# Kernel optimization log

Measured on AMD Instinct MI355X. Metric: run time of the kernel, lower is better.

The kernel has to match this reference:

```python
import jax, jax.numpy as jnp
import numpy as np

WEIGHT_BITS = 4           # weight_bit_width for both convs
SCALE_MIN = 2e-16         # scaling_min_val from CommonIntWeightPerTensorQuant


def fake_quant_per_channel(w, bits):
    """Brevitas-style per-output-channel symmetric narrow-range int fake quant.
    scale = max|w| over each output channel / (2^(bits-1) - 1), STE round."""
    qmax = float(2 ** (bits - 1) - 1)
    absmax = jnp.max(jnp.abs(w.reshape(w.shape[0], -1)), axis=1)
    scale = jnp.maximum(absmax / qmax, SCALE_MIN)
    scale = scale.reshape((-1,) + (1,) * (w.ndim - 1))
    q = jnp.clip(jnp.round(w / scale), -qmax, qmax) * scale
    # straight-through estimator (matches brevitas round_ste)
    return w + jax.lax.stop_gradient(q - w)


def setup_inputs() -> dict:
    key = jax.random.key(0)
    k1, k2, k3, k4 = jax.random.split(key, 4)
    x = jax.random.normal(k1, (32, 384, 56, 56), dtype=jnp.float32)
    # depthwise weight: (out=C, in/groups=1, kH, kW)
    dw_w = jax.random.normal(k2, (384, 1, 3, 3), dtype=jnp.float32) * 0.1
    # pointwise weight: (out, in, 1, 1); pw conv has default bias=True
    pw_w = jax.random.normal(k3, (384, 384, 1, 1), dtype=jnp.float32) * 0.05
    pw_b = jax.random.normal(k4, (384,), dtype=jnp.float32) * 0.01
    return {"x": x, "dw_w": dw_w, "pw_w": pw_w, "pw_b": pw_b}


def reference(x, dw_w, pw_w, pw_b):
    C = dw_w.shape[0]
    dw_q = fake_quant_per_channel(dw_w, WEIGHT_BITS)
    pw_q = fake_quant_per_channel(pw_w, WEIGHT_BITS)
    # depthwise 3x3, stride 1, pad 1
    y = jax.lax.conv_general_dilated(
        x, dw_q, window_strides=(1, 1), padding=((1, 1), (1, 1)),
        dimension_numbers=("NCHW", "OIHW", "NCHW"), feature_group_count=C)
    # pointwise 1x1 + bias
    z = jax.lax.conv_general_dilated(
        y, pw_q, window_strides=(1, 1), padding="VALID",
        dimension_numbers=("NCHW", "OIHW", "NCHW"))
    return z + pw_b[None, :, None, None]
```

## Files before the change

kernel.cpp:

```cpp
#include <hip/hip_runtime.h>
#include <hip/hip_bf16.h>

#define CCH 384
#define HW2 3136
#define HH 56
#define WW 56
#define QMAX 7.0f
#define SCALE_MIN 2e-16f
#define PB 49
#define YSLAB 512
#define YPB 24576

typedef _Float16 half8 __attribute__((ext_vector_type(8)));
typedef float f32x4 __attribute__((ext_vector_type(4)));

#define GLOAD_LDS16(g, l) __builtin_amdgcn_global_load_lds( \
    (const __attribute__((address_space(1))) void*)(g), \
    (__attribute__((address_space(3))) void*)(l), 16, 0, 0)


__global__ void quant_dw(const float* __restrict__ dw, float* __restrict__ dwq) {
    int c = blockIdx.x * blockDim.x + threadIdx.x;
    if (c >= CCH) return;
    float w[9];
    float amax = 0.f;
    #pragma unroll
    for (int j = 0; j < 9; ++j) {
        w[j] = dw[c * 9 + j];
        amax = fmaxf(amax, fabsf(w[j]));
    }
    float scale = fmaxf(amax / QMAX, SCALE_MIN);
    #pragma unroll
    for (int j = 0; j < 9; ++j) {
        float q = rintf(w[j] / scale);
        q = fminf(fmaxf(q, -QMAX), QMAX);
        dwq[c * 9 + j] = q * scale;
    }
}

__global__ void quant_pw(const float* __restrict__ pw, _Float16* __restrict__ wpk) {
    int co = blockIdx.x;
    int lane = threadIdx.x;
    float w[6];
    float amax = 0.f;
    #pragma unroll
    for (int j = 0; j < 6; ++j) {
        w[j] = pw[co * CCH + lane + j * 64];
        amax = fmaxf(amax, fabsf(w[j]));
    }
    #pragma unroll
    for (int off = 32; off >= 1; off >>= 1)
        amax = fmaxf(amax, __shfl_xor(amax, off));
    float scale = fmaxf(amax / QMAX, SCALE_MIN);
    #pragma unroll
    for (int j = 0; j < 6; ++j) {
        int ci = lane + j * 64;
        float q = rintf(w[j] / scale);
        q = fminf(fmaxf(q, -QMAX), QMAX);
        float v = q * scale;
        int kk  = ci >> 5;
        int cis = ci & 31;
        int l   = (co & 15) | ((cis >> 3) << 4);
        int idx = (kk * 24 + (co >> 4)) * 512 + l * 8 + (cis & 7);
        wpk[idx] = (_Float16)v;
    }
}


struct G8 { float l[8], c[8], r[8]; };

__device__ __forceinline__ void dw_load(const float* __restrict__ xc,
                                        float (&xn)[8], int srow, int wl) {
    if ((unsigned)srow < (unsigned)HH) {
        #pragma unroll
        for (int ch = 0; ch < 8; ++ch)
            xn[ch] = xc[(size_t)ch * HW2 + srow * WW + wl];
    } else {
        #pragma unroll
        for (int ch = 0; ch < 8; ++ch) xn[ch] = 0.f;
    }
}

__device__ __forceinline__ void dw_shuf(const float (&xn)[8], G8& g, int w) {
    #pragma unroll
    for (int ch = 0; ch < 8; ++ch) {
        float v = xn[ch];
        float xl = __shfl_up(v, 1);
        float xr = __shfl_down(v, 1);
        g.c[ch] = v;
        g.l[ch] = (w == 0) ? 0.f : xl;
        g.r[ch] = (w == WW - 1) ? 0.f : xr;
    }
}

__device__ __forceinline__ void dw_cs(const G8& ga, const G8& gb, const G8& gc,
                                      const float (&wq)[72], _Float16* yn,
                                      int orow, int w, bool act) {
    half8 hv;
    #pragma unroll
    for (int ch = 0; ch < 8; ++ch) {
        const int b = ch * 9;
        float a;
        a = ga.l[ch] * wq[b + 0];
        a = fmaf(ga.c[ch], wq[b + 1], a);
        a = fmaf(ga.r[ch], wq[b + 2], a);
        a = fmaf(gb.l[ch], wq[b + 3], a);
        a = fmaf(gb.c[ch], wq[b + 4], a);
        a = fmaf(gb.r[ch], wq[b + 5], a);
        a = fmaf(gc.l[ch], wq[b + 6], a);
        a = fmaf(gc.c[ch], wq[b + 7], a);
        a = fmaf(gc.r[ch], wq[b + 8], a);
        hv[ch] = (_Float16)a;
    }
    if (act) {
        const int pos = orow * WW + w;
        *(half8*)(yn + (size_t)(pos >> 6) * YPB + (pos & 63) * 8) = hv;
    }
}

#define DW_IT(K, RL, RS, GS, GA, GB, GC, DOLOAD)              \
    if (DOLOAD) dw_load(xc, RL, R0 + 3 + (K), wl);            \
    dw_shuf(RS, GS, w);                                       \
    dw_cs(GA, GB, GC, wq, yn, R0 + (K), w, act);

__global__ __launch_bounds__(128) void dw_kernel(
    const float* __restrict__ x, const float* __restrict__ dwq,
    _Float16* __restrict__ ypk)
{
    int bid = blockIdx.x;
    int wg = (bid & 7) * 384 + (bid >> 3);
    int uid = wg * 2 + (threadIdx.x >> 6);
    int quarter = uid & 3;
    int t2 = uid >> 2;
    int c8 = t2 % 48, n = t2 / 48;
    const int R0 = quarter * 14;

    const int w = threadIdx.x & 63;
    const int wl = w < WW ? w : WW - 1;
    const bool act = (w < WW);

    const float* xc = x + ((size_t)n * CCH + (size_t)c8 * 8) * HW2;
    _Float16* yn = ypk + (size_t)n * PB * YPB + (size_t)c8 * YSLAB;

    float wq[72];
    const float* wsrc = dwq + c8 * 72;
    #pragma unroll
    for (int i = 0; i < 72; ++i)
        wq[i] = __uint_as_float(
            __builtin_amdgcn_readfirstlane(__float_as_uint(wsrc[i])));

    float r0[8], r1[8], r2[8], r3[8];
    G8 g0, g1, g2;

    if (R0 == 0) {
        #pragma unroll
        for (int ch = 0; ch < 8; ++ch) r0[ch] = 0.f;
    } else {
        dw_load(xc, r0, R0 - 1, wl);
    }
    dw_load(xc, r1, R0, wl);
    dw_load(xc, r2, R0 + 1, wl);
    dw_load(xc, r3, R0 + 2, wl);
    dw_shuf(r0, g0, w);
    dw_shuf(r1, g1, w);

    DW_IT(0,  r0, r2, g2, g0, g1, g2, true)
    DW_IT(1,  r1, r3, g0, g1, g2, g0, true)
    DW_IT(2,  r2, r0, g1, g2, g0, g1, true)
    DW_IT(3,  r3, r1, g2, g0, g1, g2, true)
    DW_IT(4,  r0, r2, g0, g1, g2, g0, true)
    DW_IT(5,  r1, r3, g1, g2, g0, g1, true)
    DW_IT(6,  r2, r0, g2, g0, g1, g2, true)
    DW_IT(7,  r3, r1, g0, g1, g2, g0, true)
    DW_IT(8,  r0, r2, g1, g2, g0, g1, true)
    DW_IT(9,  r1, r3, g2, g0, g1, g2, true)
    DW_IT(10, r2, r0, g0, g1, g2, g0, true)
    DW_IT(11, r3, r1, g1, g2, g0, g1, true)
    DW_IT(12, r0, r2, g2, g0, g1, g2, false)
    DW_IT(13, r1, r3, g0, g1, g2, g0, false)
}


__global__ __launch_bounds__(256) void pw_kernel(
    const _Float16* __restrict__ ypk, const _Float16* __restrict__ wpk,
    const float* __restrict__ bias, float* __restrict__ out)
{
    __shared__ __align__(16) _Float16 ysh[YPB];

    int bid = blockIdx.x;
    int wg = (bid & 7) * 196 + (bid >> 3);
    int n = wg / PB, pb = wg % PB;

    const int t = threadIdx.x;
    const int lane = t & 63;
    const int g = __builtin_amdgcn_readfirstlane(t >> 6);

    const _Float16* yg = ypk + (size_t)(n * PB + pb) * YPB;
    #pragma unroll
    for (int j = 0; j < 12; ++j) {
        GLOAD_LDS16(yg + (j * 256 + t) * 8,
                    ysh + (size_t)(j * 256 + (t & 192)) * 8);
    }
    __syncthreads();

    const int lco = lane & 15;
    const int lkg = lane >> 4;
    const int cbf = g * 6;

    f32x4 acc[6][4];
    #pragma unroll
    for (int mc = 0; mc < 6; ++mc)
        #pragma unroll
        for (int np = 0; np < 4; ++np)
            acc[mc][np] = (f32x4){0.f, 0.f, 0.f, 0.f};

    for (int kk = 0; kk < 12; ++kk) {
        half8 wf[6];
        #pragma unroll
        for (int mc = 0; mc < 6; ++mc)
            wf[mc] = *(const half8*)(wpk + (size_t)(kk * 24 + cbf + mc) * 512 + lane * 8);
        half8 yf[4];
        #pragma unroll
        for (int np = 0; np < 4; ++np)
            yf[np] = *(const half8*)(ysh + kk * 2048 + lkg * 512 + (np * 16 + lco) * 8);
        #pragma unroll
        for (int mc = 0; mc < 6; ++mc)
            #pragma unroll
            for (int np = 0; np < 4; ++np)
                acc[mc][np] = __builtin_amdgcn_mfma_f32_16x16x32_f16(
                    wf[mc], yf[np], acc[mc][np], 0, 0, 0);
    }

    float* ob = out + (size_t)n * CCH * HW2 + (size_t)pb * 64;
    #pragma unroll
    for (int mc = 0; mc < 6; ++mc) {
        #pragma unroll
        for (int r = 0; r < 4; ++r) {
            const int co = g * 96 + mc * 16 + lkg * 4 + r;
            const float bv = bias[co];
            #pragma unroll
            for (int np = 0; np < 4; ++np)
                ob[(size_t)co * HW2 + np * 16 + lco] = acc[mc][np][r] + bv;
        }
    }
}


extern "C" void kernel_launch(void* const* d_in, const int* in_sizes, int n_in,
                              void* d_out, int out_size, void* d_ws, size_t ws_size,
                              hipStream_t stream) {
    const float* x  = (const float*)d_in[0];
    const float* dw = (const float*)d_in[1];
    const float* pw = (const float*)d_in[2];
    const float* pb = (const float*)d_in[3];
    float* out = (float*)d_out;

    float*    dwq = (float*)d_ws;
    _Float16* wpk = (_Float16*)(dwq + CCH * 9);
    _Float16* ypk = wpk + (size_t)CCH * CCH;

    quant_dw<<<2, 256, 0, stream>>>(dw, dwq);
    quant_pw<<<CCH, 64, 0, stream>>>(pw, wpk);

    dw_kernel<<<3072, 128, 0, stream>>>(x, dwq, ypk);
    pw_kernel<<<1568, 256, 0, stream>>>(ypk, wpk, pb, out);
}
```

Baseline: 117.7 us.

## Merge weight quant kernels and split depthwise work by channel halves instead of row quarters

Combines the two weight-quantization kernels into one launch to cut launch overhead. The depthwise kernel now has each wavefront handle 4 channels over 28 rows instead of 8 channels over 14 rows. This reduces halo-row reloads and register pressure per thread. In exchange, y stores become 8-byte writes interleaved between two wavefronts rather than single 16-byte stores.

```diff
diff --git a/kernel.cpp b/kernel.cpp
--- a/kernel.cpp
+++ b/kernel.cpp
@@ -12,6 +12,7 @@
 #define YPB 24576
 
 typedef _Float16 half8 __attribute__((ext_vector_type(8)));
+typedef _Float16 half4v __attribute__((ext_vector_type(4)));
 typedef float f32x4 __attribute__((ext_vector_type(4)));
 
 #define GLOAD_LDS16(g, l) __builtin_amdgcn_global_load_lds( \
@@ -19,71 +20,73 @@
     (__attribute__((address_space(3))) void*)(l), 16, 0, 0)
 
 
-__global__ void quant_dw(const float* __restrict__ dw, float* __restrict__ dwq) {
-    int c = blockIdx.x * blockDim.x + threadIdx.x;
-    if (c >= CCH) return;
-    float w[9];
-    float amax = 0.f;
-    #pragma unroll
-    for (int j = 0; j < 9; ++j) {
-        w[j] = dw[c * 9 + j];
-        amax = fmaxf(amax, fabsf(w[j]));
-    }
-    float scale = fmaxf(amax / QMAX, SCALE_MIN);
-    #pragma unroll
-    for (int j = 0; j < 9; ++j) {
-        float q = rintf(w[j] / scale);
-        q = fminf(fmaxf(q, -QMAX), QMAX);
-        dwq[c * 9 + j] = q * scale;
-    }
-}
-
-__global__ void quant_pw(const float* __restrict__ pw, _Float16* __restrict__ wpk) {
-    int co = blockIdx.x;
+__global__ void quant_all(const float* __restrict__ dw, const float* __restrict__ pw,
+                          float* __restrict__ dwq, _Float16* __restrict__ wpk) {
+    int b = blockIdx.x;
     int lane = threadIdx.x;
-    float w[6];
-    float amax = 0.f;
-    #pragma unroll
-    for (int j = 0; j < 6; ++j) {
-        w[j] = pw[co * CCH + lane + j * 64];
-        amax = fmaxf(amax, fabsf(w[j]));
-    }
-    #pragma unroll
-    for (int off = 32; off >= 1; off >>= 1)
-        amax = fmaxf(amax, __shfl_xor(amax, off));
-    float scale = fmaxf(amax / QMAX, SCALE_MIN);
-    #pragma unroll
-    for (int j = 0; j < 6; ++j) {
-        int ci = lane + j * 64;
-        float q = rintf(w[j] / scale);
-        q = fminf(fmaxf(q, -QMAX), QMAX);
-        float v = q * scale;
-        int kk  = ci >> 5;
-        int cis = ci & 31;
-        int l   = (co & 15) | ((cis >> 3) << 4);
-        int idx = (kk * 24 + (co >> 4)) * 512 + l * 8 + (cis & 7);
-        wpk[idx] = (_Float16)v;
-    }
-}
-
-
-struct G8 { float l[8], c[8], r[8]; };
+    if (b < CCH) {
+        const int co = b;
+        float w[6];
+        float amax = 0.f;
+        #pragma unroll
+        for (int j = 0; j < 6; ++j) {
+            w[j] = pw[co * CCH + lane + j * 64];
+            amax = fmaxf(amax, fabsf(w[j]));
+        }
+        #pragma unroll
+        for (int off = 32; off >= 1; off >>= 1)
+            amax = fmaxf(amax, __shfl_xor(amax, off));
+        float scale = fmaxf(amax / QMAX, SCALE_MIN);
+        #pragma unroll
+        for (int j = 0; j < 6; ++j) {
+            int ci = lane + j * 64;
+            float q = rintf(w[j] / scale);
+            q = fminf(fmaxf(q, -QMAX), QMAX);
+            float v = q * scale;
+            int kk  = ci >> 5;
+            int cis = ci & 31;
+            int l   = (co & 15) | ((cis >> 3) << 4);
+            int idx = (kk * 24 + (co >> 4)) * 512 + l * 8 + (cis & 7);
+            wpk[idx] = (_Float16)v;
+        }
+    } else {
+        const int c = (b - CCH) * 64 + lane;
+        if (c >= CCH) return;
+        float w[9];
+        float amax = 0.f;
+        #pragma unroll
+        for (int j = 0; j < 9; ++j) {
+            w[j] = dw[c * 9 + j];
+            amax = fmaxf(amax, fabsf(w[j]));
+        }
+        float scale = fmaxf(amax / QMAX, SCALE_MIN);
+        #pragma unroll
+        for (int j = 0; j < 9; ++j) {
+            float q = rintf(w[j] / scale);
+            q = fminf(fmaxf(q, -QMAX), QMAX);
+            dwq[c * 9 + j] = q * scale;
+        }
+    }
+}
+
+
+struct G4 { float l[4], c[4], r[4]; };
 
 __device__ __forceinline__ void dw_load(const float* __restrict__ xc,
-                                        float (&xn)[8], int srow, int wl) {
+                                        float (&xn)[4], int srow, int wl) {
     if ((unsigned)srow < (unsigned)HH) {
         #pragma unroll
-        for (int ch = 0; ch < 8; ++ch)
+        for (int ch = 0; ch < 4; ++ch)
             xn[ch] = xc[(size_t)ch * HW2 + srow * WW + wl];
     } else {
         #pragma unroll
-        for (int ch = 0; ch < 8; ++ch) xn[ch] = 0.f;
-    }
-}
-
-__device__ __forceinline__ void dw_shuf(const float (&xn)[8], G8& g, int w) {
-    #pragma unroll
-    for (int ch = 0; ch < 8; ++ch) {
+        for (int ch = 0; ch < 4; ++ch) xn[ch] = 0.f;
+    }
+}
+
+__device__ __forceinline__ void dw_shuf(const float (&xn)[4], G4& g, int w) {
+    #pragma unroll
+    for (int ch = 0; ch < 4; ++ch) {
         float v = xn[ch];
         float xl = __shfl_up(v, 1);
         float xr = __shfl_down(v, 1);
@@ -93,12 +96,12 @@
     }
 }
 
-__device__ __forceinline__ void dw_cs(const G8& ga, const G8& gb, const G8& gc,
-                                      const float (&wq)[72], _Float16* yn,
+__device__ __forceinline__ void dw_cs(const G4& ga, const G4& gb, const G4& gc,
+                                      const float (&wq)[36], _Float16* yn,
                                       int orow, int w, bool act) {
-    half8 hv;
-    #pragma unroll
-    for (int ch = 0; ch < 8; ++ch) {
+    half4v hv;
+    #pragma unroll
+    for (int ch = 0; ch < 4; ++ch) {
         const int b = ch * 9;
         float a;
         a = ga.l[ch] * wq[b + 0];
@@ -114,7 +117,7 @@
     }
     if (act) {
         const int pos = orow * WW + w;
-        *(half8*)(yn + (size_t)(pos >> 6) * YPB + (pos & 63) * 8) = hv;
+        *(half4v*)(yn + (size_t)(pos >> 6) * YPB + (pos & 63) * 8) = hv;
     }
 }
 
@@ -130,31 +133,32 @@
     int bid = blockIdx.x;
     int wg = (bid & 7) * 384 + (bid >> 3);
     int uid = wg * 2 + (threadIdx.x >> 6);
-    int quarter = uid & 3;
+    int chgrp = uid & 1;
+    int half = (uid >> 1) & 1;
     int t2 = uid >> 2;
     int c8 = t2 % 48, n = t2 / 48;
-    const int R0 = quarter * 14;
+    const int R0 = half * 28;
 
     const int w = threadIdx.x & 63;
     const int wl = w < WW ? w : WW - 1;
     const bool act = (w < WW);
 
-    const float* xc = x + ((size_t)n * CCH + (size_t)c8 * 8) * HW2;
-    _Float16* yn = ypk + (size_t)n * PB * YPB + (size_t)c8 * YSLAB;
-
-    float wq[72];
-    const float* wsrc = dwq + c8 * 72;
-    #pragma unroll
-    for (int i = 0; i < 72; ++i)
+    const float* xc = x + ((size_t)n * CCH + (size_t)c8 * 8 + chgrp * 4) * HW2;
+    _Float16* yn = ypk + (size_t)n * PB * YPB + (size_t)c8 * YSLAB + chgrp * 4;
+
+    float wq[36];
+    const float* wsrc = dwq + (c8 * 8 + chgrp * 4) * 9;
+    #pragma unroll
+    for (int i = 0; i < 36; ++i)
         wq[i] = __uint_as_float(
             __builtin_amdgcn_readfirstlane(__float_as_uint(wsrc[i])));
 
-    float r0[8], r1[8], r2[8], r3[8];
-    G8 g0, g1, g2;
+    float r0[4], r1[4], r2[4], r3[4];
+    G4 g0, g1, g2;
 
     if (R0 == 0) {
         #pragma unroll
-        for (int ch = 0; ch < 8; ++ch) r0[ch] = 0.f;
+        for (int ch = 0; ch < 4; ++ch) r0[ch] = 0.f;
     } else {
         dw_load(xc, r0, R0 - 1, wl);
     }
@@ -176,8 +180,22 @@
     DW_IT(9,  r1, r3, g2, g0, g1, g2, true)
     DW_IT(10, r2, r0, g0, g1, g2, g0, true)
     DW_IT(11, r3, r1, g1, g2, g0, g1, true)
-    DW_IT(12, r0, r2, g2, g0, g1, g2, false)
-    DW_IT(13, r1, r3, g0, g1, g2, g0, false)
+    DW_IT(12, r0, r2, g2, g0, g1, g2, true)
+    DW_IT(13, r1, r3, g0, g1, g2, g0, true)
+    DW_IT(14, r2, r0, g1, g2, g0, g1, true)
+    DW_IT(15, r3, r1, g2, g0, g1, g2, true)
+    DW_IT(16, r0, r2, g0, g1, g2, g0, true)
+    DW_IT(17, r1, r3, g1, g2, g0, g1, true)
+    DW_IT(18, r2, r0, g2, g0, g1, g2, true)
+    DW_IT(19, r3, r1, g0, g1, g2, g0, true)
+    DW_IT(20, r0, r2, g1, g2, g0, g1, true)
+    DW_IT(21, r1, r3, g2, g0, g1, g2, true)
+    DW_IT(22, r2, r0, g0, g1, g2, g0, true)
+    DW_IT(23, r3, r1, g1, g2, g0, g1, true)
+    DW_IT(24, r0, r2, g2, g0, g1, g2, true)
+    DW_IT(25, r1, r3, g0, g1, g2, g0, true)
+    DW_IT(26, r2, r0, g1, g2, g0, g1, false)
+    DW_IT(27, r3, r1, g2, g0, g1, g2, false)
 }
 
 
@@ -259,8 +277,7 @@
     _Float16* wpk = (_Float16*)(dwq + CCH * 9);
     _Float16* ypk = wpk + (size_t)CCH * CCH;
 
-    quant_dw<<<2, 256, 0, stream>>>(dw, dwq);
-    quant_pw<<<CCH, 64, 0, stream>>>(pw, wpk);
+    quant_all<<<CCH + 6, 64, 0, stream>>>(dw, pw, dwq, wpk);
 
     dw_kernel<<<3072, 128, 0, stream>>>(x, dwq, ypk);
     pw_kernel<<<1568, 256, 0, stream>>>(ypk, wpk, pb, out);
```

Result: slower. 120.1 us (+2.1%).
